# Kernel optimization log

Measured on AMD Instinct MI355X. Metric: run time of the kernel, lower is better.

Reference implementation:

```python
import jax, jax.numpy as jnp
import numpy as np

N = 20000
E = 400000
D = 128  # latent_dim


def _bce(p, t):
    # torch F.binary_cross_entropy clamps log terms at -100
    logp = jnp.clip(jnp.log(p), -100.0)
    log1mp = jnp.clip(jnp.log(1.0 - p), -100.0)
    return -jnp.mean(t * logp + (1.0 - t) * log1mp)


def setup_inputs() -> dict:
    key = jax.random.key(0)
    ks = jax.random.split(key, 12)
    pos = jax.random.normal(ks[0], (N,), jnp.float32)
    s = jax.random.uniform(ks[1], (N,), dtype=jnp.float32)
    edge_index = jax.random.randint(ks[2], (2, E), 0, N)
    pi = jax.random.randint(ks[3], (E,), 0, 2)
    pi_h = jax.random.randint(ks[4], (4, E), 0, 2)
    reach_h = jax.random.randint(ks[5], (4, N), 0, 2)
    sc = 0.1
    W_enc = sc * jax.random.normal(ks[6], (2, D), jnp.float32)
    b_enc = jnp.zeros((D,), jnp.float32)
    W_msg = sc * jax.random.normal(ks[7], (2 * D, D), jnp.float32)
    b_msg = jnp.zeros((D,), jnp.float32)
    W_self = sc * jax.random.normal(ks[8], (2 * D, D), jnp.float32)
    W_agg = sc * jax.random.normal(ks[9], (D, D), jnp.float32)
    b_upd = jnp.zeros((D,), jnp.float32)
    W_dec = sc * jax.random.normal(ks[10], (2 * D, 1), jnp.float32)
    b_dec = jnp.zeros((1,), jnp.float32)
    return dict(pos=pos, s=s, edge_index=edge_index, pi=pi, pi_h=pi_h, reach_h=reach_h,
                W_enc=W_enc, b_enc=b_enc, W_msg=W_msg, b_msg=b_msg,
                W_self=W_self, W_agg=W_agg, b_upd=b_upd, W_dec=W_dec, b_dec=b_dec)


def reference(pos, s, edge_index, pi, pi_h, reach_h,
              W_enc, b_enc, W_msg, b_msg, W_self, W_agg, b_upd, W_dec, b_dec):
    n = pos.shape[0]
    src, dst = edge_index[0], edge_index[1]
    idx_both = jnp.concatenate([src, dst])  # incident-edge readout indices
    hints = pi_h[1:].astype(jnp.float32)              # [T, E]
    hints_reach = reach_h[1:].astype(jnp.float32)     # [T, N]
    max_iter = hints.shape[0] + 1

    h = jnp.zeros((n, D), jnp.float32)
    sfeat = s
    preds, preds_y = [], []
    for _ in range(max_iter):  # small fixed iteration count (algorithm steps)
        inp = jnp.stack([pos, sfeat], axis=1)                      # [N, 2]
        z = jax.nn.relu(inp @ W_enc + b_enc)                       # encoder
        x = jnp.concatenate([z, h], axis=1)                        # [N, 2D]
        msg = jax.nn.relu(x[src] @ W_msg + b_msg)                  # [E, D]
        agg = jax.ops.segment_max(msg, dst, num_segments=n)        # scatter-max
        agg = jnp.where(jnp.isfinite(agg), agg, 0.0)
        h = jax.nn.relu(x @ W_self + agg @ W_agg + b_upd)          # processor
        ef = jnp.concatenate([h[src], h[dst]], axis=1)             # [E, 2D]
        alpha = jax.nn.sigmoid(ef @ W_dec + b_dec)[:, 0]           # decoder -> per-edge prob
        preds.append(alpha)
        # per-node max over all incident edges (both endpoints), threshold 0.8
        amax = jax.ops.segment_max(jnp.concatenate([alpha, alpha]), idx_both, num_segments=n)
        y = (amax >= 0.8).astype(jnp.float32)
        preds_y.append(y)
        sfeat = y

    predictions = jnp.stack(preds)        # [max_iter, E]
    predictions_y = jnp.stack(preds_y)    # [max_iter, N]

    loss_x = _bce(predictions[-1], pi.astype(jnp.float32))
    loss_h = jnp.asarray(0.0, jnp.float32)
    for i in range(hints.shape[0]):
        loss_h = loss_h + _bce(predictions[i], hints[i])
    y_loss_x = _bce(predictions_y[-1], reach_h[-1].astype(jnp.float32))
    y_loss_h = jnp.asarray(0.0, jnp.float32)
    for i in range(hints_reach.shape[0]):
        y_loss_h = y_loss_h + _bce(predictions_y[i], hints_reach[i])
    return (y, loss_x, loss_h, y_loss_x, y_loss_h)
```

## Files before the change

### kernel.cpp

```cpp
#include <hip/hip_runtime.h>

#define CSR_B 128

__global__ __launch_bounds__(256) void k_hist2(const int* __restrict__ eidx, int E, int N,
                                               int* __restrict__ partial_d,
                                               int* __restrict__ partial_s) {
  extern __shared__ unsigned int hist[];
  int nw = (N + 1) >> 1;
  for (int i = threadIdx.x; i < 2 * nw; i += blockDim.x) hist[i] = 0u;
  __syncthreads();
  const int* src = eidx;
  const int* dst = eidx + E;
  int chunk = (E + CSR_B - 1) / CSR_B;
  int beg = blockIdx.x * chunk, end = min(E, beg + chunk);
  for (int e = beg + threadIdx.x; e < end; e += blockDim.x) {
    int d = dst[e];
    atomicAdd(&hist[d >> 1], 1u << ((d & 1) * 16));
    int s = src[e];
    atomicAdd(&hist[nw + (s >> 1)], 1u << ((s & 1) * 16));
  }
  __syncthreads();
  for (int i = threadIdx.x; i < N; i += blockDim.x) {
    partial_d[(size_t)blockIdx.x * N + i] = (int)((hist[i >> 1] >> ((i & 1) * 16)) & 0xFFFFu);
    partial_s[(size_t)blockIdx.x * N + i] = (int)((hist[nw + (i >> 1)] >> ((i & 1) * 16)) & 0xFFFFu);
  }
}

__global__ __launch_bounds__(256) void k_colscan2(int* __restrict__ partial_d,
                                                  int* __restrict__ cnt_d,
                                                  int* __restrict__ partial_s,
                                                  int* __restrict__ cnt_s, int N) {
  int g = blockIdx.x * blockDim.x + threadIdx.x;
  int* partial;
  int* cnt;
  int bin;
  if (g < N) { partial = partial_d; cnt = cnt_d; bin = g; }
  else if (g < 2 * N) { partial = partial_s; cnt = cnt_s; bin = g - N; }
  else return;
  int run = 0;
  for (int b = 0; b < CSR_B; ++b) {
    int t = partial[(size_t)b * N + bin];
    partial[(size_t)b * N + bin] = run;
    run += t;
  }
  cnt[bin] = run;
}

__device__ __forceinline__ void scan_one(const int* __restrict__ cnt, int* __restrict__ rp,
                                         int N, int* sums) {
  int t = threadIdx.x;
  int chunk = (N + 1023) / 1024;
  int beg = t * chunk, end = min(N, beg + chunk);
  int s = 0;
  for (int i = beg; i < end; ++i) s += cnt[i];
  sums[t] = s;
  __syncthreads();
  for (int off = 1; off < 1024; off <<= 1) {
    int v = (t >= off) ? sums[t - off] : 0;
    __syncthreads();
    sums[t] += v;
    __syncthreads();
  }
  int run = (t > 0) ? sums[t - 1] : 0;
  if (t == 0) rp[0] = 0;
  for (int i = beg; i < end; ++i) { run += cnt[i]; rp[i + 1] = run; }
}

__global__ __launch_bounds__(1024) void k_scan2both(const int* __restrict__ cnt_d,
                                                    int* __restrict__ rp_d,
                                                    const int* __restrict__ cnt_s,
                                                    int* __restrict__ rp_s, int N) {
  __shared__ int sums[1024];
  scan_one(cnt_d, rp_d, N, sums);
  __syncthreads();
  scan_one(cnt_s, rp_s, N, sums);
}

__global__ __launch_bounds__(256) void k_scatter2(
    const int* __restrict__ eidx, int E, int N,
    const int* __restrict__ partial_d, const int* __restrict__ rp_d, int* __restrict__ csr_src,
    const int* __restrict__ partial_s, const int* __restrict__ rp_s, int* __restrict__ csr_dst) {
  extern __shared__ unsigned int cur[];
  int nw = (N + 1) >> 1;
  for (int i = threadIdx.x; i < 2 * nw; i += blockDim.x) cur[i] = 0u;
  __syncthreads();
  const int* src = eidx;
  const int* dst = eidx + E;
  int chunk = (E + CSR_B - 1) / CSR_B;
  int beg = blockIdx.x * chunk, end = min(E, beg + chunk);
  for (int e = beg + threadIdx.x; e < end; e += blockDim.x) {
    int d = dst[e], s = src[e];
    int shd = (d & 1) * 16;
    unsigned int old = atomicAdd(&cur[d >> 1], 1u << shd);
    csr_src[rp_d[d] + partial_d[(size_t)blockIdx.x * N + d] + (int)((old >> shd) & 0xFFFFu)] = s;
    int shs = (s & 1) * 16;
    unsigned int old2 = atomicAdd(&cur[nw + (s >> 1)], 1u << shs);
    csr_dst[rp_s[s] + partial_s[(size_t)blockIdx.x * N + s] + (int)((old2 >> shs) & 0xFFFFu)] = d;
  }
}

__global__ void k_build_w(const float* __restrict__ W_msg, const float* __restrict__ W_self,
                          const float* __restrict__ b_msg, float* __restrict__ Wcat,
                          float* __restrict__ bcat) {
  int idx = blockIdx.x * blockDim.x + threadIdx.x;
  int k = idx >> 8, j = idx & 255;
  Wcat[idx] = (j < 128) ? W_msg[k * 128 + j] : W_self[k * 128 + (j - 128)];
  if (idx < 256) bcat[idx] = (idx < 128) ? b_msg[idx] : 0.0f;
}

__device__ __forceinline__ float4 enc4(float p, float sf, float4 we0, float4 we1, float4 be) {
  float4 r;
  r.x = fmaxf(fmaf(p, we0.x, fmaf(sf, we1.x, be.x)), 0.f);
  r.y = fmaxf(fmaf(p, we0.y, fmaf(sf, we1.y, be.y)), 0.f);
  r.z = fmaxf(fmaf(p, we0.z, fmaf(sf, we1.z, be.z)), 0.f);
  r.w = fmaxf(fmaf(p, we0.w, fmaf(sf, we1.w, be.w)), 0.f);
  return r;
}

template <bool IT0>
__global__ __launch_bounds__(512) void k_gemm(
    const float* __restrict__ pos, const float* __restrict__ sfeat,
    const float* __restrict__ hsrc, const float* __restrict__ W_enc,
    const float* __restrict__ b_enc, const float* __restrict__ B,
    const float* __restrict__ bias, float* __restrict__ C, int M) {
  __shared__ float As[16][132];
  __shared__ float Bs[16][64];
  const int m0 = blockIdx.x * 128, n0 = blockIdx.y * 64;
  const int t = threadIdx.x;
  const int ty = t >> 4, tx = t & 15;
  const int lr = t >> 2, lq = (t & 3) << 2;
  const int row_ld = m0 + lr;
  const bool valid = row_ld < M;
  float p = 0.f, sf = 0.f;
  if (valid) { p = pos[row_ld]; sf = sfeat[row_ld]; }
  const int bk = t >> 4, bc = (t & 15) << 2;
  float acc[4][4] = {};
  const int KMAX = IT0 ? 128 : 256;
  for (int k0 = 0; k0 < KMAX; k0 += 16) {
    const int col = k0 + lq;
    float4 av = make_float4(0.f, 0.f, 0.f, 0.f);
    if (valid) {
      if (col < 128) {
        float4 we0 = *reinterpret_cast<const float4*>(&W_enc[col]);
        float4 we1 = *reinterpret_cast<const float4*>(&W_enc[128 + col]);
        float4 be = *reinterpret_cast<const float4*>(&b_enc[col]);
        av = enc4(p, sf, we0, we1, be);
      } else {
        av = *reinterpret_cast<const float4*>(&hsrc[(size_t)row_ld * 128 + col - 128]);
      }
    }
    As[lq + 0][lr] = av.x;
    As[lq + 1][lr] = av.y;
    As[lq + 2][lr] = av.z;
    As[lq + 3][lr] = av.w;
    if (t < 256)
      *reinterpret_cast<float4*>(&Bs[bk][bc]) =
          *reinterpret_cast<const float4*>(&B[(size_t)(k0 + bk) * 256 + n0 + bc]);
    __syncthreads();
#pragma unroll
    for (int k = 0; k < 16; ++k) {
      float4 a4 = *reinterpret_cast<const float4*>(&As[k][ty * 4]);
      float4 b4 = *reinterpret_cast<const float4*>(&Bs[k][tx * 4]);
      const float a[4] = {a4.x, a4.y, a4.z, a4.w};
      const float b[4] = {b4.x, b4.y, b4.z, b4.w};
#pragma unroll
      for (int i = 0; i < 4; ++i)
#pragma unroll
        for (int j = 0; j < 4; ++j) acc[i][j] = fmaf(a[i], b[j], acc[i][j]);
    }
    __syncthreads();
  }
  float4 b4 = *reinterpret_cast<const float4*>(&bias[n0 + tx * 4]);
#pragma unroll
  for (int i = 0; i < 4; ++i) {
    int row = m0 + ty * 4 + i;
    if (row < M) {
      float4 o = make_float4(acc[i][0] + b4.x, acc[i][1] + b4.y, acc[i][2] + b4.z,
                             acc[i][3] + b4.w);
      *reinterpret_cast<float4*>(&C[(size_t)row * 256 + n0 + tx * 4]) = o;
    }
  }
}

__global__ __launch_bounds__(256) void k_aggmax(
    const float* __restrict__ xw, const int* __restrict__ row_ptr,
    const int* __restrict__ csr_src, float* __restrict__ agg, int N, int Nh) {
  const int cx = blockIdx.x & 7;
  const int chunk = cx & 3;
  const int half = cx >> 2;
  const int hw = threadIdx.x >> 5;
  const int sub = threadIdx.x & 31;
  const int node = half * Nh + blockIdx.y * 8 + hw;
  const int hi = half ? N : Nh;
  if (node >= hi) return;
  const float* base = xw + chunk * 32 + sub;
  const int beg = row_ptr[node], end = row_ptr[node + 1];
  float m0 = 0.f, m1 = 0.f, m2 = 0.f, m3 = 0.f;
  int i = beg;
  for (; i + 3 < end; i += 4) {
    int e0 = csr_src[i], e1 = csr_src[i + 1], e2 = csr_src[i + 2], e3 = csr_src[i + 3];
    float f0 = base[(size_t)e0 * 256];
    float f1 = base[(size_t)e1 * 256];
    float f2 = base[(size_t)e2 * 256];
    float f3 = base[(size_t)e3 * 256];
    m0 = fmaxf(m0, f0); m1 = fmaxf(m1, f1);
    m2 = fmaxf(m2, f2); m3 = fmaxf(m3, f3);
  }
  for (; i < end; ++i) m0 = fmaxf(m0, base[(size_t)csr_src[i] * 256]);
  m0 = fmaxf(fmaxf(m0, m1), fmaxf(m2, m3));
  agg[(size_t)node * 128 + chunk * 32 + sub] = m0;
}

__global__ __launch_bounds__(256) void k_update2(
    const float* __restrict__ agg, const float* __restrict__ W_agg,
    const float* __restrict__ b_upd, const float* __restrict__ xw,
    const float* __restrict__ W_dec, const float* __restrict__ b_dec,
    float* __restrict__ h, float* __restrict__ u, float* __restrict__ v, int M) {
  __shared__ float As[32][33];
  __shared__ float Bs[32][128];
  const int m0 = blockIdx.x * 32;
  const int t = threadIdx.x;
  const int ty = t >> 5, tx = t & 31;
  const int lar = t >> 3, lac = (t & 7) << 2;
  float acc[4][4] = {};
  for (int k0 = 0; k0 < 128; k0 += 32) {
    {
      float4 av = make_float4(0.f, 0.f, 0.f, 0.f);
      int row = m0 + lar;
      if (row < M) av = *reinterpret_cast<const float4*>(&agg[(size_t)row * 128 + k0 + lac]);
      As[lar][lac + 0] = av.x;
      As[lar][lac + 1] = av.y;
      As[lar][lac + 2] = av.z;
      As[lar][lac + 3] = av.w;
#pragma unroll
      for (int p = 0; p < 4; ++p) {
        int br = (t >> 5) + p * 8;
        *reinterpret_cast<float4*>(&Bs[br][tx * 4]) =
            *reinterpret_cast<const float4*>(&W_agg[(size_t)(k0 + br) * 128 + tx * 4]);
      }
    }
    __syncthreads();
#pragma unroll
    for (int k = 0; k < 32; ++k) {
      float4 b4 = *reinterpret_cast<const float4*>(&Bs[k][tx * 4]);
      const float bb[4] = {b4.x, b4.y, b4.z, b4.w};
#pragma unroll
      for (int j = 0; j < 4; ++j) {
        float a = As[ty * 4 + j][k];
#pragma unroll
        for (int c = 0; c < 4; ++c) acc[j][c] = fmaf(a, bb[c], acc[j][c]);
      }
    }
    __syncthreads();
  }
  const float4 bu4 = *reinterpret_cast<const float4*>(&b_upd[tx * 4]);
  const float4 wdu = *reinterpret_cast<const float4*>(&W_dec[tx * 4]);
  const float4 wdv = *reinterpret_cast<const float4*>(&W_dec[128 + tx * 4]);
  const float bd = b_dec[0];
#pragma unroll
  for (int j = 0; j < 4; ++j) {
    int row = m0 + ty * 4 + j;
    if (row >= M) continue;
    float4 sf = *reinterpret_cast<const float4*>(&xw[(size_t)row * 256 + 128 + tx * 4]);
    float4 h4;
    h4.x = fmaxf(acc[j][0] + sf.x + bu4.x, 0.f);
    h4.y = fmaxf(acc[j][1] + sf.y + bu4.y, 0.f);
    h4.z = fmaxf(acc[j][2] + sf.z + bu4.z, 0.f);
    h4.w = fmaxf(acc[j][3] + sf.w + bu4.w, 0.f);
    *reinterpret_cast<float4*>(&h[(size_t)row * 128 + tx * 4]) = h4;
    float up = h4.x * wdu.x + h4.y * wdu.y + h4.z * wdu.z + h4.w * wdu.w;
    float vp = h4.x * wdv.x + h4.y * wdv.y + h4.z * wdv.z + h4.w * wdv.w;
#pragma unroll
    for (int m = 16; m > 0; m >>= 1) {
      up += __shfl_xor(up, m);
      vp += __shfl_xor(vp, m);
    }
    if (tx == 0) {
      u[row] = up + bd;
      v[row] = vp;
    }
  }
}

#define GB 512
__global__ __launch_bounds__(256) void k_losses(
    const int* __restrict__ src, const int* __restrict__ dst, const float* __restrict__ u,
    const float* __restrict__ v, const int* __restrict__ tgt, const int* __restrict__ row_ptr,
    const int* __restrict__ csr_src, const int* __restrict__ row_ptr2,
    const int* __restrict__ csr_dst, const int* __restrict__ reach_row,
    float* __restrict__ ybuf, float* __restrict__ yout, int write_out,
    double* __restrict__ pe_slot, double* __restrict__ py_slot, int E, int N) {
  __shared__ double wsum[4];
  double term = 0.0;
  for (int e = blockIdx.x * blockDim.x + threadIdx.x; e < E; e += GB * 256) {
    float l = u[src[e]] + v[dst[e]];
    float a = 1.0f / (1.0f + expf(-l));
    float t = (float)tgt[e];
    float lp = fmaxf(logf(a), -100.0f);
    float l1 = fmaxf(logf(1.0f - a), -100.0f);
    term += (double)(t * lp + (1.0f - t) * l1);
  }
#pragma unroll
  for (int off = 32; off > 0; off >>= 1) term += __shfl_down(term, off);
  if ((threadIdx.x & 63) == 0) wsum[threadIdx.x >> 6] = term;
  __syncthreads();
  if (threadIdx.x == 0) pe_slot[blockIdx.x] = wsum[0] + wsum[1] + wsum[2] + wsum[3];
  __syncthreads();
  double c = 0.0;
  for (int n = blockIdx.x * blockDim.x + threadIdx.x; n < N; n += GB * 256) {
    float mu = -INFINITY, mv = -INFINITY;
    const int b1 = row_ptr[n], e1 = row_ptr[n + 1];
    for (int i = b1; i < e1; ++i) mu = fmaxf(mu, u[csr_src[i]]);
    const int b2 = row_ptr2[n], e2 = row_ptr2[n + 1];
    for (int i = b2; i < e2; ++i) mv = fmaxf(mv, v[csr_dst[i]]);
    float m = fmaxf(mu + v[n], u[n] + mv);
    float a = 1.0f / (1.0f + expf(-m));
    float yv = (a >= 0.8f) ? 1.0f : 0.0f;
    ybuf[n] = yv;
    if (write_out) yout[n] = yv;
    if ((float)reach_row[n] != yv) c = 100.0;
  }
#pragma unroll
  for (int off = 32; off > 0; off >>= 1) c += __shfl_down(c, off);
  if ((threadIdx.x & 63) == 0) wsum[threadIdx.x >> 6] = c;
  __syncthreads();
  if (threadIdx.x == 0) py_slot[blockIdx.x] = wsum[0] + wsum[1] + wsum[2] + wsum[3];
}

__global__ void k_final(const double* __restrict__ pe, const double* __restrict__ py,
                        float* __restrict__ out4, int N, int E, int T) {
  __shared__ double le[8], ly[8];
  int lane = threadIdx.x;
  for (int it = 0; it < T; ++it) {
    double s = 0.0;
    for (int i = lane; i < GB; i += 64) s += pe[(size_t)it * GB + i];
#pragma unroll
    for (int off = 32; off > 0; off >>= 1) s += __shfl_down(s, off);
    if (lane == 0) le[it] = s;
    double s2 = 0.0;
    for (int i = lane; i < GB; i += 64) s2 += py[(size_t)it * GB + i];
#pragma unroll
    for (int off = 32; off > 0; off >>= 1) s2 += __shfl_down(s2, off);
    if (lane == 0) ly[it] = s2;
  }
  __syncthreads();
  if (lane == 0) {
    float loss_x = (float)(-le[T - 1] / (double)E);
    float loss_h = 0.0f;
    for (int i = 0; i < T - 1; ++i) loss_h += (float)(-le[i] / (double)E);
    float yl_x = (float)(ly[T - 1] / (double)N);
    float yl_h = 0.0f;
    for (int i = 0; i < T - 1; ++i) yl_h += (float)(ly[i] / (double)N);
    out4[0] = loss_x;
    out4[1] = loss_h;
    out4[2] = yl_x;
    out4[3] = yl_h;
  }
}

extern "C" void kernel_launch(void* const* d_in, const int* in_sizes, int n_in,
                              void* d_out, int out_size, void* d_ws, size_t ws_size,
                              hipStream_t stream) {
  const float* pos = (const float*)d_in[0];
  const float* s = (const float*)d_in[1];
  const int* eidx = (const int*)d_in[2];
  const int* pi = (const int*)d_in[3];
  const int* pi_h = (const int*)d_in[4];
  const int* reach = (const int*)d_in[5];
  const float* W_enc = (const float*)d_in[6];
  const float* b_enc = (const float*)d_in[7];
  const float* W_msg = (const float*)d_in[8];
  const float* b_msg = (const float*)d_in[9];
  const float* W_self = (const float*)d_in[10];
  const float* W_agg = (const float*)d_in[11];
  const float* b_upd = (const float*)d_in[12];
  const float* W_dec = (const float*)d_in[13];
  const float* b_dec = (const float*)d_in[14];

  const int N = in_sizes[0];
  const int E = in_sizes[3];
  const int T = in_sizes[4] / in_sizes[3];
  const int* src = eidx;
  const int* dst = eidx + E;

  char* w = (char*)d_ws;
  auto alloc = [&](size_t bytes) {
    char* p = w;
    w += (bytes + 255) & ~(size_t)255;
    return p;
  };
  float* xw = (float*)alloc((size_t)N * 256 * 4);
  float* agg = (float*)alloc((size_t)N * 128 * 4);
  float* h = (float*)alloc((size_t)N * 128 * 4);
  float* Wcat = (float*)alloc(256 * 256 * 4);
  float* bcat = (float*)alloc(256 * 4);
  float* u = (float*)alloc((size_t)N * 4);
  float* v = (float*)alloc((size_t)N * 4);
  float* ybuf = (float*)alloc((size_t)N * 4);
  int* cnt_d = (int*)alloc((size_t)N * 4);
  int* cnt_s = (int*)alloc((size_t)N * 4);
  int* row_ptr = (int*)alloc((size_t)(N + 1) * 4);
  int* row_ptr2 = (int*)alloc((size_t)(N + 1) * 4);
  int* csr_src = (int*)alloc((size_t)E * 4);
  int* csr_dst = (int*)alloc((size_t)E * 4);
  int* partial_d = (int*)alloc((size_t)CSR_B * N * 4);
  int* partial_s = (int*)alloc((size_t)CSR_B * N * 4);
  double* pe = (double*)alloc((size_t)T * GB * 8);
  double* py = (double*)alloc((size_t)T * GB * 8);

  float* outy = (float*)d_out;
  float* out4 = outy + N;

  k_build_w<<<256, 256, 0, stream>>>(W_msg, W_self, b_msg, Wcat, bcat);

  const size_t lds2 = (size_t)2 * ((N + 1) >> 1) * 4;
  k_hist2<<<CSR_B, 256, lds2, stream>>>(eidx, E, N, partial_d, partial_s);
  k_colscan2<<<(2 * N + 255) / 256, 256, 0, stream>>>(partial_d, cnt_d, partial_s, cnt_s, N);
  k_scan2both<<<1, 1024, 0, stream>>>(cnt_d, row_ptr, cnt_s, row_ptr2, N);
  k_scatter2<<<CSR_B, 256, lds2, stream>>>(eidx, E, N, partial_d, row_ptr, csr_src, partial_s,
                                           row_ptr2, csr_dst);

  const int Nh = (N + 1) / 2;
  const int NB = (Nh + 7) / 8;

  const float* sfeat = s;
  for (int it = 0; it < T; ++it) {
    dim3 g1((N + 127) / 128, 4);
    if (it == 0)
      k_gemm<true><<<g1, 512, 0, stream>>>(pos, sfeat, h, W_enc, b_enc, Wcat, bcat, xw, N);
    else
      k_gemm<false><<<g1, 512, 0, stream>>>(pos, sfeat, h, W_enc, b_enc, Wcat, bcat, xw, N);

    k_aggmax<<<dim3(8, NB), 256, 0, stream>>>(xw, row_ptr, csr_src, agg, N, Nh);

    k_update2<<<(N + 31) / 32, 256, 0, stream>>>(agg, W_agg, b_upd, xw, W_dec, b_dec,
                                                 h, u, v, N);

    const int* tgt = (it < T - 1) ? (pi_h + (size_t)(it + 1) * E) : pi;
    const int* rrow = (it < T - 1) ? (reach + (size_t)(it + 1) * N) : (reach + (size_t)(T - 1) * N);
    k_losses<<<GB, 256, 0, stream>>>(src, dst, u, v, tgt, row_ptr, csr_src, row_ptr2, csr_dst,
                                     rrow, ybuf, outy, (it == T - 1) ? 1 : 0,
                                     pe + (size_t)it * GB, py + (size_t)it * GB, E, N);
    sfeat = ybuf;
  }
  k_final<<<1, 64, 0, stream>>>(pe, py, out4, N, E, T);
}
```

Measured before the change: 547.0 us.

## Retile node GEMM to 64x128 blocks with 8x8 register tiles per thread

Restructures the encoder+message/self GEMM so each 128-thread block computes a 64x128 output tile, with each thread holding an 8x8 (2x2 of 4x4) accumulator tile instead of 4x4. The aim is higher arithmetic intensity per shared-memory load and less redundant recomputation of the encoder input across column blocks (grid y drops from 4 to 2). In exchange it uses more registers per thread and launches fewer, smaller blocks, which may lower occupancy and latency hiding.

```diff
diff --git a/kernel.cpp b/kernel.cpp
--- a/kernel.cpp
+++ b/kernel.cpp
@@ -118,67 +118,88 @@
 }
 
 template <bool IT0>
-__global__ __launch_bounds__(512) void k_gemm(
+__global__ __launch_bounds__(128) void k_gemm(
     const float* __restrict__ pos, const float* __restrict__ sfeat,
     const float* __restrict__ hsrc, const float* __restrict__ W_enc,
     const float* __restrict__ b_enc, const float* __restrict__ B,
     const float* __restrict__ bias, float* __restrict__ C, int M) {
-  __shared__ float As[16][132];
-  __shared__ float Bs[16][64];
-  const int m0 = blockIdx.x * 128, n0 = blockIdx.y * 64;
+  __shared__ float As[16][68];
+  __shared__ float Bs[16][132];
+  const int m0 = blockIdx.x * 64, n0 = blockIdx.y * 128;
   const int t = threadIdx.x;
   const int ty = t >> 4, tx = t & 15;
-  const int lr = t >> 2, lq = (t & 3) << 2;
+  const int lr = t >> 1, cq = (t & 1) << 3;
   const int row_ld = m0 + lr;
   const bool valid = row_ld < M;
   float p = 0.f, sf = 0.f;
   if (valid) { p = pos[row_ld]; sf = sfeat[row_ld]; }
-  const int bk = t >> 4, bc = (t & 15) << 2;
-  float acc[4][4] = {};
+  const int bc = (t & 31) << 2, br0 = t >> 5;
+  float acc[2][2][4][4] = {};
   const int KMAX = IT0 ? 128 : 256;
   for (int k0 = 0; k0 < KMAX; k0 += 16) {
-    const int col = k0 + lq;
-    float4 av = make_float4(0.f, 0.f, 0.f, 0.f);
+    const int col = k0 + cq;
+    float4 a0 = make_float4(0.f, 0.f, 0.f, 0.f), a1 = a0;
     if (valid) {
       if (col < 128) {
         float4 we0 = *reinterpret_cast<const float4*>(&W_enc[col]);
         float4 we1 = *reinterpret_cast<const float4*>(&W_enc[128 + col]);
-        float4 be = *reinterpret_cast<const float4*>(&b_enc[col]);
-        av = enc4(p, sf, we0, we1, be);
+        float4 be  = *reinterpret_cast<const float4*>(&b_enc[col]);
+        a0 = enc4(p, sf, we0, we1, be);
+        we0 = *reinterpret_cast<const float4*>(&W_enc[col + 4]);
+        we1 = *reinterpret_cast<const float4*>(&W_enc[128 + col + 4]);
+        be  = *reinterpret_cast<const float4*>(&b_enc[col + 4]);
+        a1 = enc4(p, sf, we0, we1, be);
       } else {
-        av = *reinterpret_cast<const float4*>(&hsrc[(size_t)row_ld * 128 + col - 128]);
+        a0 = *reinterpret_cast<const float4*>(&hsrc[(size_t)row_ld * 128 + col - 128]);
+        a1 = *reinterpret_cast<const float4*>(&hsrc[(size_t)row_ld * 128 + col - 124]);
       }
     }
-    As[lq + 0][lr] = av.x;
-    As[lq + 1][lr] = av.y;
-    As[lq + 2][lr] = av.z;
-    As[lq + 3][lr] = av.w;
-    if (t < 256)
-      *reinterpret_cast<float4*>(&Bs[bk][bc]) =
-          *reinterpret_cast<const float4*>(&B[(size_t)(k0 + bk) * 256 + n0 + bc]);
+    As[cq + 0][lr] = a0.x; As[cq + 1][lr] = a0.y;
+    As[cq + 2][lr] = a0.z; As[cq + 3][lr] = a0.w;
+    As[cq + 4][lr] = a1.x; As[cq + 5][lr] = a1.y;
+    As[cq + 6][lr] = a1.z; As[cq + 7][lr] = a1.w;
+#pragma unroll
+    for (int pp = 0; pp < 4; ++pp) {
+      int br = br0 + pp * 4;
+      *reinterpret_cast<float4*>(&Bs[br][bc]) =
+          *reinterpret_cast<const float4*>(&B[(size_t)(k0 + br) * 256 + n0 + bc]);
+    }
     __syncthreads();
 #pragma unroll
     for (int k = 0; k < 16; ++k) {
-      float4 a4 = *reinterpret_cast<const float4*>(&As[k][ty * 4]);
-      float4 b4 = *reinterpret_cast<const float4*>(&Bs[k][tx * 4]);
-      const float a[4] = {a4.x, a4.y, a4.z, a4.w};
-      const float b[4] = {b4.x, b4.y, b4.z, b4.w};
-#pragma unroll
-      for (int i = 0; i < 4; ++i)
-#pragma unroll
-        for (int j = 0; j < 4; ++j) acc[i][j] = fmaf(a[i], b[j], acc[i][j]);
-    }
-    __syncthreads();
-  }
-  float4 b4 = *reinterpret_cast<const float4*>(&bias[n0 + tx * 4]);
-#pragma unroll
-  for (int i = 0; i < 4; ++i) {
-    int row = m0 + ty * 4 + i;
-    if (row < M) {
-      float4 o = make_float4(acc[i][0] + b4.x, acc[i][1] + b4.y, acc[i][2] + b4.z,
-                             acc[i][3] + b4.w);
-      *reinterpret_cast<float4*>(&C[(size_t)row * 256 + n0 + tx * 4]) = o;
-    }
+      float4 alo = *reinterpret_cast<const float4*>(&As[k][ty * 4]);
+      float4 ahi = *reinterpret_cast<const float4*>(&As[k][32 + ty * 4]);
+      float4 blo = *reinterpret_cast<const float4*>(&Bs[k][tx * 4]);
+      float4 bhi = *reinterpret_cast<const float4*>(&Bs[k][64 + tx * 4]);
+      const float av[2][4] = {{alo.x, alo.y, alo.z, alo.w}, {ahi.x, ahi.y, ahi.z, ahi.w}};
+      const float bv[2][4] = {{blo.x, blo.y, blo.z, blo.w}, {bhi.x, bhi.y, bhi.z, bhi.w}};
+#pragma unroll
+      for (int ih = 0; ih < 2; ++ih)
+#pragma unroll
+        for (int jh = 0; jh < 2; ++jh)
+#pragma unroll
+          for (int i = 0; i < 4; ++i)
+#pragma unroll
+            for (int j = 0; j < 4; ++j)
+              acc[ih][jh][i][j] = fmaf(av[ih][i], bv[jh][j], acc[ih][jh][i][j]);
+    }
+    __syncthreads();
+  }
+#pragma unroll
+  for (int jh = 0; jh < 2; ++jh) {
+    const int colb = n0 + jh * 64 + tx * 4;
+    float4 b4 = *reinterpret_cast<const float4*>(&bias[colb]);
+#pragma unroll
+    for (int ih = 0; ih < 2; ++ih)
+#pragma unroll
+      for (int i = 0; i < 4; ++i) {
+        int row = m0 + ih * 32 + ty * 4 + i;
+        if (row < M) {
+          float4 o = make_float4(acc[ih][jh][i][0] + b4.x, acc[ih][jh][i][1] + b4.y,
+                                 acc[ih][jh][i][2] + b4.z, acc[ih][jh][i][3] + b4.w);
+          *reinterpret_cast<float4*>(&C[(size_t)row * 256 + colb]) = o;
+        }
+      }
   }
 }
 
@@ -425,11 +446,11 @@
 
   const float* sfeat = s;
   for (int it = 0; it < T; ++it) {
-    dim3 g1((N + 127) / 128, 4);
+    dim3 g1((N + 63) / 64, 2);
     if (it == 0)
-      k_gemm<true><<<g1, 512, 0, stream>>>(pos, sfeat, h, W_enc, b_enc, Wcat, bcat, xw, N);
+      k_gemm<true><<<g1, 128, 0, stream>>>(pos, sfeat, h, W_enc, b_enc, Wcat, bcat, xw, N);
     else
-      k_gemm<false><<<g1, 512, 0, stream>>>(pos, sfeat, h, W_enc, b_enc, Wcat, bcat, xw, N);
+      k_gemm<false><<<g1, 128, 0, stream>>>(pos, sfeat, h, W_enc, b_enc, Wcat, bcat, xw, N);
 
     k_aggmax<<<dim3(8, NB), 256, 0, stream>>>(xw, row_ptr, csr_src, agg, N, Nh);
 
```

Result: slower. 574.2 us (+5.0%).

## Split encoder out and rewrite node GEMM with register-tiled A loads and full-K LDS B

Applied to the files above, without the earlier changes.

The encoder is moved into its own kernel, which writes z into a persistent [N,256] x buffer. The update kernel now writes h straight into the second half of that buffer, so the GEMM reads a plain contiguous A. The GEMM is rewritten to keep the whole K-slice of B in LDS and to stream A rows from global memory into registers with double buffering, which removes the per-k-tile syncs and the A staging in LDS. The update kernel also transposes its A tile so each thread reads a float4 per k instead of four scalars. The costs are an extra kernel launch per iteration, extra global traffic for x, and uncoalesced per-thread row loads of A in the GEMM.

```diff
diff --git a/kernel.cpp b/kernel.cpp
--- a/kernel.cpp
+++ b/kernel.cpp
@@ -108,76 +108,80 @@
   if (idx < 256) bcat[idx] = (idx < 128) ? b_msg[idx] : 0.0f;
 }
 
-__device__ __forceinline__ float4 enc4(float p, float sf, float4 we0, float4 we1, float4 be) {
-  float4 r;
-  r.x = fmaxf(fmaf(p, we0.x, fmaf(sf, we1.x, be.x)), 0.f);
-  r.y = fmaxf(fmaf(p, we0.y, fmaf(sf, we1.y, be.y)), 0.f);
-  r.z = fmaxf(fmaf(p, we0.z, fmaf(sf, we1.z, be.z)), 0.f);
-  r.w = fmaxf(fmaf(p, we0.w, fmaf(sf, we1.w, be.w)), 0.f);
-  return r;
-}
-
-template <bool IT0>
-__global__ __launch_bounds__(512) void k_gemm(
+__global__ __launch_bounds__(256) void k_encode(
     const float* __restrict__ pos, const float* __restrict__ sfeat,
-    const float* __restrict__ hsrc, const float* __restrict__ W_enc,
-    const float* __restrict__ b_enc, const float* __restrict__ B,
+    const float* __restrict__ W_enc, const float* __restrict__ b_enc,
+    float* __restrict__ x, int N) {
+  int idx = blockIdx.x * blockDim.x + threadIdx.x;
+  int n = idx >> 5, d4 = (idx & 31) << 2;
+  if (n >= N) return;
+  float p = pos[n], sf = sfeat[n];
+  float4 we0 = *reinterpret_cast<const float4*>(&W_enc[d4]);
+  float4 we1 = *reinterpret_cast<const float4*>(&W_enc[128 + d4]);
+  float4 be  = *reinterpret_cast<const float4*>(&b_enc[d4]);
+  float4 z;
+  z.x = fmaxf(fmaf(p, we0.x, fmaf(sf, we1.x, be.x)), 0.f);
+  z.y = fmaxf(fmaf(p, we0.y, fmaf(sf, we1.y, be.y)), 0.f);
+  z.z = fmaxf(fmaf(p, we0.z, fmaf(sf, we1.z, be.z)), 0.f);
+  z.w = fmaxf(fmaf(p, we0.w, fmaf(sf, we1.w, be.w)), 0.f);
+  *reinterpret_cast<float4*>(&x[(size_t)n * 256 + d4]) = z;
+}
+
+template <int KT>
+__global__ __launch_bounds__(256) void k_gemm_nb(
+    const float* __restrict__ x, const float* __restrict__ B,
     const float* __restrict__ bias, float* __restrict__ C, int M) {
-  __shared__ float As[16][132];
-  __shared__ float Bs[16][64];
+  __shared__ float Bs[KT][64];
   const int m0 = blockIdx.x * 128, n0 = blockIdx.y * 64;
   const int t = threadIdx.x;
-  const int ty = t >> 4, tx = t & 15;
-  const int lr = t >> 2, lq = (t & 3) << 2;
-  const int row_ld = m0 + lr;
-  const bool valid = row_ld < M;
-  float p = 0.f, sf = 0.f;
-  if (valid) { p = pos[row_ld]; sf = sfeat[row_ld]; }
-  const int bk = t >> 4, bc = (t & 15) << 2;
-  float acc[4][4] = {};
-  const int KMAX = IT0 ? 128 : 256;
-  for (int k0 = 0; k0 < KMAX; k0 += 16) {
-    const int col = k0 + lq;
-    float4 av = make_float4(0.f, 0.f, 0.f, 0.f);
-    if (valid) {
-      if (col < 128) {
-        float4 we0 = *reinterpret_cast<const float4*>(&W_enc[col]);
-        float4 we1 = *reinterpret_cast<const float4*>(&W_enc[128 + col]);
-        float4 be = *reinterpret_cast<const float4*>(&b_enc[col]);
-        av = enc4(p, sf, we0, we1, be);
-      } else {
-        av = *reinterpret_cast<const float4*>(&hsrc[(size_t)row_ld * 128 + col - 128]);
-      }
-    }
-    As[lq + 0][lr] = av.x;
-    As[lq + 1][lr] = av.y;
-    As[lq + 2][lr] = av.z;
-    As[lq + 3][lr] = av.w;
-    if (t < 256)
-      *reinterpret_cast<float4*>(&Bs[bk][bc]) =
-          *reinterpret_cast<const float4*>(&B[(size_t)(k0 + bk) * 256 + n0 + bc]);
-    __syncthreads();
-#pragma unroll
-    for (int k = 0; k < 16; ++k) {
-      float4 a4 = *reinterpret_cast<const float4*>(&As[k][ty * 4]);
-      float4 b4 = *reinterpret_cast<const float4*>(&Bs[k][tx * 4]);
-      const float a[4] = {a4.x, a4.y, a4.z, a4.w};
-      const float b[4] = {b4.x, b4.y, b4.z, b4.w};
-#pragma unroll
-      for (int i = 0; i < 4; ++i)
-#pragma unroll
-        for (int j = 0; j < 4; ++j) acc[i][j] = fmaf(a[i], b[j], acc[i][j]);
-    }
-    __syncthreads();
-  }
-  float4 b4 = *reinterpret_cast<const float4*>(&bias[n0 + tx * 4]);
-#pragma unroll
-  for (int i = 0; i < 4; ++i) {
-    int row = m0 + ty * 4 + i;
+  for (int idx = t; idx < KT * 16; idx += 256) {
+    int row = idx >> 4, c4 = (idx & 15) << 2;
+    *reinterpret_cast<float4*>(&Bs[row][c4]) =
+        *reinterpret_cast<const float4*>(&B[(size_t)row * 256 + n0 + c4]);
+  }
+  __syncthreads();
+
+  const int c4 = (t & 15) << 2;
+  const int r0 = m0 + (t >> 4) * 8;
+  int rows[8];
+#pragma unroll
+  for (int i = 0; i < 8; ++i) rows[i] = min(r0 + i, M - 1);
+
+  float4 a_[8], b_[8];
+  float acc[8][4] = {};
+#define LOADA(buf, kk)                                                                \
+  _Pragma("unroll") for (int i = 0; i < 8; ++i) buf[i] =                              \
+      *reinterpret_cast<const float4*>(&x[(size_t)rows[i] * 256 + (kk)]);
+#define COMP(buf, kk)                                                                 \
+  _Pragma("unroll") for (int j = 0; j < 4; ++j) {                                     \
+    float4 b4 = *reinterpret_cast<const float4*>(&Bs[(kk) + j][c4]);                  \
+    _Pragma("unroll") for (int i = 0; i < 8; ++i) {                                   \
+      float av = (j == 0) ? buf[i].x : (j == 1) ? buf[i].y : (j == 2) ? buf[i].z      \
+                                                                      : buf[i].w;     \
+      acc[i][0] = fmaf(av, b4.x, acc[i][0]);                                          \
+      acc[i][1] = fmaf(av, b4.y, acc[i][1]);                                          \
+      acc[i][2] = fmaf(av, b4.z, acc[i][2]);                                          \
+      acc[i][3] = fmaf(av, b4.w, acc[i][3]);                                          \
+    }                                                                                 \
+  }
+
+  LOADA(a_, 0);
+  for (int k0 = 0; k0 < KT; k0 += 8) {
+    LOADA(b_, k0 + 4);
+    COMP(a_, k0);
+    if (k0 + 8 < KT) { LOADA(a_, k0 + 8); }
+    COMP(b_, k0 + 4);
+  }
+#undef LOADA
+#undef COMP
+  float4 bi = *reinterpret_cast<const float4*>(&bias[n0 + c4]);
+#pragma unroll
+  for (int i = 0; i < 8; ++i) {
+    int row = r0 + i;
     if (row < M) {
-      float4 o = make_float4(acc[i][0] + b4.x, acc[i][1] + b4.y, acc[i][2] + b4.z,
-                             acc[i][3] + b4.w);
-      *reinterpret_cast<float4*>(&C[(size_t)row * 256 + n0 + tx * 4]) = o;
+      float4 o = make_float4(acc[i][0] + bi.x, acc[i][1] + bi.y, acc[i][2] + bi.z,
+                             acc[i][3] + bi.w);
+      *reinterpret_cast<float4*>(&C[(size_t)row * 256 + n0 + c4]) = o;
     }
   }
 }
@@ -215,8 +219,8 @@
     const float* __restrict__ agg, const float* __restrict__ W_agg,
     const float* __restrict__ b_upd, const float* __restrict__ xw,
     const float* __restrict__ W_dec, const float* __restrict__ b_dec,
-    float* __restrict__ h, float* __restrict__ u, float* __restrict__ v, int M) {
-  __shared__ float As[32][33];
+    float* __restrict__ x, float* __restrict__ u, float* __restrict__ v, int M) {
+  __shared__ float AsT[32][33];
   __shared__ float Bs[32][128];
   const int m0 = blockIdx.x * 32;
   const int t = threadIdx.x;
@@ -228,10 +232,10 @@
       float4 av = make_float4(0.f, 0.f, 0.f, 0.f);
       int row = m0 + lar;
       if (row < M) av = *reinterpret_cast<const float4*>(&agg[(size_t)row * 128 + k0 + lac]);
-      As[lar][lac + 0] = av.x;
-      As[lar][lac + 1] = av.y;
-      As[lar][lac + 2] = av.z;
-      As[lar][lac + 3] = av.w;
+      AsT[lac + 0][lar] = av.x;
+      AsT[lac + 1][lar] = av.y;
+      AsT[lac + 2][lar] = av.z;
+      AsT[lac + 3][lar] = av.w;
 #pragma unroll
       for (int p = 0; p < 4; ++p) {
         int br = (t >> 5) + p * 8;
@@ -242,14 +246,14 @@
     __syncthreads();
 #pragma unroll
     for (int k = 0; k < 32; ++k) {
+      float4 a4 = *reinterpret_cast<const float4*>(&AsT[k][ty * 4]);
       float4 b4 = *reinterpret_cast<const float4*>(&Bs[k][tx * 4]);
+      const float aa[4] = {a4.x, a4.y, a4.z, a4.w};
       const float bb[4] = {b4.x, b4.y, b4.z, b4.w};
 #pragma unroll
-      for (int j = 0; j < 4; ++j) {
-        float a = As[ty * 4 + j][k];
-#pragma unroll
-        for (int c = 0; c < 4; ++c) acc[j][c] = fmaf(a, bb[c], acc[j][c]);
-      }
+      for (int j = 0; j < 4; ++j)
+#pragma unroll
+        for (int c = 0; c < 4; ++c) acc[j][c] = fmaf(aa[j], bb[c], acc[j][c]);
     }
     __syncthreads();
   }
@@ -267,7 +271,7 @@
     h4.y = fmaxf(acc[j][1] + sf.y + bu4.y, 0.f);
     h4.z = fmaxf(acc[j][2] + sf.z + bu4.z, 0.f);
     h4.w = fmaxf(acc[j][3] + sf.w + bu4.w, 0.f);
-    *reinterpret_cast<float4*>(&h[(size_t)row * 128 + tx * 4]) = h4;
+    *reinterpret_cast<float4*>(&x[(size_t)row * 256 + 128 + tx * 4]) = h4;
     float up = h4.x * wdu.x + h4.y * wdu.y + h4.z * wdu.z + h4.w * wdu.w;
     float vp = h4.x * wdv.x + h4.y * wdv.y + h4.z * wdv.z + h4.w * wdv.w;
 #pragma unroll
@@ -389,9 +393,9 @@
     w += (bytes + 255) & ~(size_t)255;
     return p;
   };
+  float* x = (float*)alloc((size_t)N * 256 * 4);
   float* xw = (float*)alloc((size_t)N * 256 * 4);
   float* agg = (float*)alloc((size_t)N * 128 * 4);
-  float* h = (float*)alloc((size_t)N * 128 * 4);
   float* Wcat = (float*)alloc(256 * 256 * 4);
   float* bcat = (float*)alloc(256 * 4);
   float* u = (float*)alloc((size_t)N * 4);
@@ -425,16 +429,18 @@
 
   const float* sfeat = s;
   for (int it = 0; it < T; ++it) {
+    k_encode<<<(N * 32 + 255) / 256, 256, 0, stream>>>(pos, sfeat, W_enc, b_enc, x, N);
+
     dim3 g1((N + 127) / 128, 4);
     if (it == 0)
-      k_gemm<true><<<g1, 512, 0, stream>>>(pos, sfeat, h, W_enc, b_enc, Wcat, bcat, xw, N);
+      k_gemm_nb<128><<<g1, 256, 0, stream>>>(x, Wcat, bcat, xw, N);
     else
-      k_gemm<false><<<g1, 512, 0, stream>>>(pos, sfeat, h, W_enc, b_enc, Wcat, bcat, xw, N);
+      k_gemm_nb<256><<<g1, 256, 0, stream>>>(x, Wcat, bcat, xw, N);
 
     k_aggmax<<<dim3(8, NB), 256, 0, stream>>>(xw, row_ptr, csr_src, agg, N, Nh);
 
     k_update2<<<(N + 31) / 32, 256, 0, stream>>>(agg, W_agg, b_upd, xw, W_dec, b_dec,
-                                                 h, u, v, N);
+                                                 x, u, v, N);
 
     const int* tgt = (it < T - 1) ? (pi_h + (size_t)(it + 1) * E) : pi;
     const int* rrow = (it < T - 1) ? (reach + (size_t)(it + 1) * N) : (reach + (size_t)(T - 1) * N);
```

New measurement: 1.265 ms. 131% more time.
